# Kernel optimization log

Measured on AMD Instinct MI355X. Metric: run time of the kernel, lower is better.

The kernel has to match this reference:

```python
import jax, jax.numpy as jnp
import numpy as np

B, N, D, H, DK, DV, HID, L = 64, 512, 128, 8, 16, 16, 512, 3


def _attention(xq, xk, xv, Wq, Wk, Wv, Wo, mask=None):
    b, nq, _ = xq.shape
    nk = xk.shape[1]
    dk = Wq.shape[1] // H
    dv = Wv.shape[1] // H
    qs = (xq @ Wq).reshape(b, nq, H, dk).transpose(0, 2, 1, 3)   # [b,H,nq,dk]
    ks = (xk @ Wk).reshape(b, nk, H, dk).transpose(0, 2, 1, 3)   # [b,H,nk,dk]
    vs = (xv @ Wv).reshape(b, nk, H, dv).transpose(0, 2, 1, 3)   # [b,H,nk,dv]
    u = jnp.einsum('bhqd,bhkd->bhqk', qs, ks) / (float(dk) ** 0.5)
    if mask is not None:
        u = jnp.where(mask[:, None, None, :], -jnp.inf, u)
    a = jax.nn.softmax(u, axis=-1)
    att = jnp.einsum('bhqk,bhkd->bhqd', a, vs).transpose(0, 2, 1, 3).reshape(b, nq, H * dv)
    return att @ Wo


def _ln(x, g, b):
    mu = x.mean(-1, keepdims=True)
    var = ((x - mu) ** 2).mean(-1, keepdims=True)
    return (x - mu) / jnp.sqrt(var + 1e-6) * g + b


def setup_inputs() -> dict:
    key = jax.random.key(0)
    ks = jax.random.split(key, 32)
    s = 0.02
    def rn(k, shape):
        return jax.random.normal(k, shape, jnp.float32) * s
    return {
        'problems': jax.random.normal(ks[0], (B, N, 2), jnp.float32),
        'embed_W': rn(ks[1], (2, D)),
        'embed_b': jnp.zeros((D,), jnp.float32),
        'enc_Wq': rn(ks[2], (L, D, H * DK)),
        'enc_Wk': rn(ks[3], (L, D, H * DK)),
        'enc_Wv': rn(ks[4], (L, D, H * DV)),
        'enc_Wo': rn(ks[5], (L, H * DV, D)),
        'enc_ln1_g': jnp.ones((L, D), jnp.float32),
        'enc_ln1_b': jnp.zeros((L, D), jnp.float32),
        'enc_ff_W1': rn(ks[6], (L, D, HID)),
        'enc_ff_b1': jnp.zeros((L, HID), jnp.float32),
        'enc_ff_W2': rn(ks[7], (L, HID, D)),
        'enc_ff_b2': jnp.zeros((L, D), jnp.float32),
        'enc_ln2_g': jnp.ones((L, D), jnp.float32),
        'enc_ln2_b': jnp.zeros((L, D), jnp.float32),
        'graph_W': rn(ks[8], (D, D)),
        'node_W': rn(ks[9], (D, D)),
        'dec_Wq': rn(ks[10], (3 * D, H * DK)),
        'dec_Wk': rn(ks[11], (D, H * DK)),
        'dec_Wv': rn(ks[12], (D, H * DV)),
        'dec_Wo': rn(ks[13], (H * DV, D)),
        'W_v_f': jax.random.uniform(ks[14], (1, 1, D), jnp.float32),
        'W_v_l': jax.random.uniform(ks[15], (1, 1, D), jnp.float32),
    }


def reference(problems, embed_W, embed_b, enc_Wq, enc_Wk, enc_Wv, enc_Wo,
              enc_ln1_g, enc_ln1_b, enc_ff_W1, enc_ff_b1, enc_ff_W2, enc_ff_b2,
              enc_ln2_g, enc_ln2_b, graph_W, node_W,
              dec_Wq, dec_Wk, dec_Wv, dec_Wo, W_v_f, W_v_l):
    # --- encoder ---
    x = problems @ embed_W + embed_b
    for i in range(L):
        x = _ln(x + _attention(x, x, x, enc_Wq[i], enc_Wk[i], enc_Wv[i], enc_Wo[i]),
                enc_ln1_g[i], enc_ln1_b[i])
        h = jax.nn.relu(x @ enc_ff_W1[i] + enc_ff_b1[i]) @ enc_ff_W2[i] + enc_ff_b2[i]
        x = _ln(x + h, enc_ln2_g[i], enc_ln2_b[i])
    node_context = x                                             # [B,N,D]
    graph_context = node_context.mean(axis=1, keepdims=True) @ graph_W  # [B,1,D]
    k_node = node_context @ node_W                               # loop-invariant, hoisted
    first0 = jnp.broadcast_to(W_v_f, (B, 1, D))
    last0 = jnp.broadcast_to(W_v_l, (B, 1, D))
    mask0 = jnp.zeros((B, N), bool)
    step_keys = jax.random.split(jax.random.key(42), N)
    batch_idx = jnp.arange(B)

    def step(carry, inp):
        mask, last, first = carry
        i, k = inp
        cq = jnp.concatenate([graph_context, last, first], axis=-1)   # [B,1,3D]
        q = _attention(cq, node_context, node_context, dec_Wq, dec_Wk, dec_Wv, dec_Wo, mask)  # [B,1,D]
        logits = jnp.einsum('bqd,bnd->bqn', q, k_node)[:, 0, :] / (float(D) ** 0.5)
        logits = jnp.where(mask, -jnp.inf, jnp.tanh(logits) * 10.0)
        actions = jax.random.categorical(k, logits)                   # [B]
        probs = jax.nn.softmax(logits, axis=-1)
        p = jnp.take_along_axis(probs, actions[:, None], axis=1)[:, 0]
        mask = mask.at[batch_idx, actions].set(True)
        # faithful to original: gather index is [1,B,D], so it reads batch 0's node_context
        new_last = node_context[0][actions][:, None, :]               # [B,1,D]
        first = jnp.where(i == 0, new_last, first)
        return (mask, new_last, first), (p, actions)

    _, (probs_seq, actions_seq) = jax.lax.scan(
        step, (mask0, last0, first0), (jnp.arange(N), step_keys))
    return probs_seq, actions_seq
```

## Files before the change

### kernel.cpp

```cpp
#include <hip/hip_runtime.h>


#define NEGINF (-__builtin_huge_valf())
#define TINYF 1.17549435e-38f

__device__ __forceinline__ unsigned rotl32(unsigned v, int r) {
  return (v << r) | (v >> (32 - r));
}

__device__ __forceinline__ void threefry2x32(unsigned k0, unsigned k1,
                                             unsigned& x0, unsigned& x1) {
  unsigned k2 = k0 ^ k1 ^ 0x1BD11BDAu;
  x0 += k0; x1 += k1;
#define TF_R(r) { x0 += x1; x1 = rotl32(x1, (r)); x1 ^= x0; }
  TF_R(13) TF_R(15) TF_R(26) TF_R(6)
  x0 += k1; x1 += k2 + 1u;
  TF_R(17) TF_R(29) TF_R(16) TF_R(24)
  x0 += k2; x1 += k0 + 2u;
  TF_R(13) TF_R(15) TF_R(26) TF_R(6)
  x0 += k0; x1 += k1 + 3u;
  TF_R(17) TF_R(29) TF_R(16) TF_R(24)
  x0 += k1; x1 += k2 + 4u;
  TF_R(13) TF_R(15) TF_R(26) TF_R(6)
  x0 += k2; x1 += k0 + 5u;
#undef TF_R
}

__device__ __forceinline__ float4 f4fma(float s, float4 v, float4 a) {
  a.x += s * v.x; a.y += s * v.y; a.z += s * v.z; a.w += s * v.w; return a;
}

__global__ __launch_bounds__(256) void k_embed(const float* __restrict__ P,
                                               const float* __restrict__ eW,
                                               const float* __restrict__ eb,
                                               float* __restrict__ X) {
  int idx = blockIdx.x * 256 + threadIdx.x;
  int row = idx >> 7, d = idx & 127;
  X[idx] = P[row * 2] * eW[d] + P[row * 2 + 1] * eW[128 + d] + eb[d];
}

__global__ __launch_bounds__(256) void k_gemm128(const float* __restrict__ A,
                                                 const float* __restrict__ W,
                                                 const float* __restrict__ R,
                                                 float* __restrict__ C, int M) {
  __shared__ float As[16][129];
  __shared__ float Ws[128][17];
  const int tx = threadIdx.x & 15, ty = threadIdx.x >> 4;
  const int row0 = blockIdx.x * 16, col0 = blockIdx.y * 16;
  for (int idx = threadIdx.x; idx < 2048; idx += 256) {
    int r = idx >> 7, k = idx & 127;
    As[r][k] = (row0 + r < M) ? A[(size_t)(row0 + r) * 128 + k] : 0.0f;
    int kk = idx >> 4, c = idx & 15;
    Ws[kk][c] = W[(size_t)kk * 128 + col0 + c];
  }
  __syncthreads();
  float acc = 0.0f;
#pragma unroll 8
  for (int k = 0; k < 128; ++k) acc += As[ty][k] * Ws[k][tx];
  const int row = row0 + ty, col = col0 + tx;
  if (row < M) {
    if (R) acc += R[(size_t)row * 128 + col];
    C[(size_t)row * 128 + col] = acc;
  }
}

#define GEP_BIAS 1
#define GEP_RELU 2
#define GEP_ADDR 4
#define GEP_ACC  8
#define GEP_TST  16
#define GEP_WT   32

__global__ __launch_bounds__(256, 2) void k_gemm64(
    const float* __restrict__ A, int lda,
    const float* __restrict__ W, int ldw,
    const float* __restrict__ bias,
    const float* __restrict__ R,
    float* __restrict__ C, int ldc,
    int K, int flags) {
  __shared__ float AsT[128 * 68];
  __shared__ float Bs[128 * 68];
  const int t = threadIdx.x;
  const int tx = t & 15, ty = t >> 4;
  const int row0 = blockIdx.x * 64, col0 = blockIdx.y * 64;
  float4 acc[4];
  acc[0] = acc[1] = acc[2] = acc[3] = make_float4(0.f, 0.f, 0.f, 0.f);

  for (int K0 = 0; K0 < K; K0 += 128) {
    if (K0) __syncthreads();
#pragma unroll
    for (int j = 0; j < 8; ++j) {
      int idx = t + j * 256;
      int r = idx & 63, kq = idx >> 6;
      float4 v = *(const float4*)&A[(size_t)(row0 + r) * lda + K0 + kq * 4];
      AsT[(kq * 4 + 0) * 68 + r] = v.x;
      AsT[(kq * 4 + 1) * 68 + r] = v.y;
      AsT[(kq * 4 + 2) * 68 + r] = v.z;
      AsT[(kq * 4 + 3) * 68 + r] = v.w;
    }
    if (flags & GEP_WT) {
#pragma unroll
      for (int j = 0; j < 8; ++j) {
        int idx = t + j * 256;
        int cc = idx & 63, kq = idx >> 6;
        float4 v = *(const float4*)&W[(size_t)(col0 + cc) * ldw + K0 + kq * 4];
        Bs[(kq * 4 + 0) * 68 + cc] = v.x;
        Bs[(kq * 4 + 1) * 68 + cc] = v.y;
        Bs[(kq * 4 + 2) * 68 + cc] = v.z;
        Bs[(kq * 4 + 3) * 68 + cc] = v.w;
      }
    } else {
#pragma unroll
      for (int j = 0; j < 8; ++j) {
        int idx = t + j * 256;
        int c4 = idx & 15, k = idx >> 4;
        *(float4*)&Bs[k * 68 + c4 * 4] =
            *(const float4*)&W[(size_t)(K0 + k) * ldw + col0 + c4 * 4];
      }
    }
    __syncthreads();
#pragma unroll 8
    for (int k = 0; k < 128; ++k) {
      float4 av = *(const float4*)&AsT[k * 68 + ty * 4];
      float4 bv = *(const float4*)&Bs[k * 68 + tx * 4];
      acc[0] = f4fma(av.x, bv, acc[0]);
      acc[1] = f4fma(av.y, bv, acc[1]);
      acc[2] = f4fma(av.z, bv, acc[2]);
      acc[3] = f4fma(av.w, bv, acc[3]);
    }
  }

  if (flags & GEP_TST) {
    __syncthreads();
    float* CtT = AsT;
#pragma unroll
    for (int i2 = 0; i2 < 4; ++i2) {
      CtT[(tx * 4 + 0) * 68 + ty * 4 + i2] = ((const float*)&acc[i2])[0];
      CtT[(tx * 4 + 1) * 68 + ty * 4 + i2] = ((const float*)&acc[i2])[1];
      CtT[(tx * 4 + 2) * 68 + ty * 4 + i2] = ((const float*)&acc[i2])[2];
      CtT[(tx * 4 + 3) * 68 + ty * 4 + i2] = ((const float*)&acc[i2])[3];
    }
    __syncthreads();
    for (int j = 0; j < 16; ++j) {
      int idx = t + j * 256;
      int n = idx & 63, c = idx >> 6;
      int grow = row0 + n;
      C[(size_t)(grow >> 9) * 65536 + (size_t)(col0 + c) * 512 + (grow & 511)] =
          CtT[c * 68 + n];
    }
  } else {
#pragma unroll
    for (int i2 = 0; i2 < 4; ++i2) {
      const int row = row0 + ty * 4 + i2, col = col0 + tx * 4;
      float4 v = acc[i2];
      if (flags & GEP_BIAS) {
        float4 b4 = *(const float4*)&bias[col];
        v.x += b4.x; v.y += b4.y; v.z += b4.z; v.w += b4.w;
      }
      if (flags & GEP_RELU) {
        v.x = fmaxf(v.x, 0.f); v.y = fmaxf(v.y, 0.f);
        v.z = fmaxf(v.z, 0.f); v.w = fmaxf(v.w, 0.f);
      }
      if (flags & GEP_ADDR) {
        float4 r4 = *(const float4*)&R[(size_t)row * ldc + col];
        v.x += r4.x; v.y += r4.y; v.z += r4.z; v.w += r4.w;
      }
      if (flags & GEP_ACC) {
        float4 c4 = *(const float4*)&C[(size_t)row * ldc + col];
        v.x += c4.x; v.y += c4.y; v.z += c4.z; v.w += c4.w;
      }
      *(float4*)&C[(size_t)row * ldc + col] = v;
    }
  }
}

__global__ __launch_bounds__(512, 2) void k_attn_enc(const float* __restrict__ Q,
                                                     const float* __restrict__ K,
                                                     const float* __restrict__ V,
                                                     float* __restrict__ O) {
  const int b = blockIdx.x >> 3, h = blockIdx.x & 7;
  const int t = threadIdx.x, l = t & 63, w = t >> 6;
  __shared__ float4 Vs4[512][5];
  __shared__ float S[32][516];
  __shared__ float Qs[32][16];
  __shared__ float invr[32];
  const size_t base = (size_t)b * 512 * 128 + (size_t)h * 16;
  float4 k0, k1, k2, k3;
  {
    const float4* kr = reinterpret_cast<const float4*>(K + base + (size_t)t * 128);
    k0 = kr[0]; k1 = kr[1]; k2 = kr[2]; k3 = kr[3];
  }
  for (int idx = t; idx < 2048; idx += 512) {
    int n = idx >> 2, c = idx & 3;
    Vs4[n][c] = reinterpret_cast<const float4*>(V + base + (size_t)n * 128)[c];
  }
  __syncthreads();
  const float* vsf = reinterpret_cast<const float*>(Vs4);
  for (int qt = 0; qt < 16; ++qt) {
    { int qr = t >> 4, d = t & 15;
      Qs[qr][d] = Q[base + (size_t)(qt * 32 + qr) * 128 + d]; }
    __syncthreads();
#pragma unroll 4
    for (int qi = 0; qi < 32; ++qi) {
      const float* qv = Qs[qi];
      float s = qv[0] * k0.x + qv[1] * k0.y + qv[2] * k0.z + qv[3] * k0.w
              + qv[4] * k1.x + qv[5] * k1.y + qv[6] * k1.z + qv[7] * k1.w
              + qv[8] * k2.x + qv[9] * k2.y + qv[10] * k2.z + qv[11] * k2.w
              + qv[12] * k3.x + qv[13] * k3.y + qv[14] * k3.z + qv[15] * k3.w;
      S[qi][t] = s * 0.25f;
    }
    __syncthreads();
    for (int r = 0; r < 4; ++r) {
      const int qi = w * 4 + r;
      float m = S[qi][l];
      for (int j = 1; j < 8; ++j) m = fmaxf(m, S[qi][l + 64 * j]);
      for (int o = 32; o; o >>= 1) m = fmaxf(m, __shfl_xor(m, o));
      float sum = 0.0f;
      for (int j = 0; j < 8; ++j) {
        float e = expf(S[qi][l + 64 * j] - m);
        S[qi][l + 64 * j] = e;
        sum += e;
      }
      for (int o = 32; o; o >>= 1) sum += __shfl_xor(sum, o);
      if (l == 0) invr[qi] = 1.0f / sum;
    }
    __syncthreads();
    {
      const int qi = t >> 4, d = t & 15;
      float acc = 0.0f;
      for (int n = 0; n < 512; ++n) acc += S[qi][n] * vsf[n * 20 + d];
      O[base + (size_t)(qt * 32 + qi) * 128 + d] = acc * invr[qi];
    }
  }
}

__global__ __launch_bounds__(256) void k_ln(const float* __restrict__ Y,
                                            const float* __restrict__ g,
                                            const float* __restrict__ bb,
                                            float* __restrict__ O, int M) {
  const int row = blockIdx.x * 4 + (threadIdx.x >> 6);
  const int l = threadIdx.x & 63;
  if (row >= M) return;
  const float* y = Y + (size_t)row * 128;
  float v0 = y[l], v1 = y[l + 64];
  float s = v0 + v1;
  for (int o = 32; o; o >>= 1) s += __shfl_xor(s, o);
  const float mu = s * (1.0f / 128.0f);
  float d0 = v0 - mu, d1 = v1 - mu;
  float q = d0 * d0 + d1 * d1;
  for (int o = 32; o; o >>= 1) q += __shfl_xor(q, o);
  const float sd = sqrtf(q * (1.0f / 128.0f) + 1e-6f);
  O[(size_t)row * 128 + l]      = d0 / sd * g[l] + bb[l];
  O[(size_t)row * 128 + l + 64] = d1 / sd * g[l + 64] + bb[l + 64];
}

__global__ __launch_bounds__(128) void k_mean(const float* __restrict__ X,
                                              float* __restrict__ NM) {
  const int b = blockIdx.x, d = threadIdx.x;
  float s = 0.0f;
  for (int n = 0; n < 512; ++n) s += X[((size_t)b * 512 + n) * 128 + d];
  NM[b * 128 + d] = s * (1.0f / 512.0f);
}

__global__ __launch_bounds__(512, 2) void k_decoder(
    const float* __restrict__ Kt, const float* __restrict__ Vt,
    const float* __restrict__ KnWT,
    const float* __restrict__ QG, const float* __restrict__ QL,
    const float* __restrict__ QF, const float* __restrict__ QL0,
    const float* __restrict__ QF0,
    float* __restrict__ out_probs, float* __restrict__ out_act) {
  const int b = blockIdx.x, t = threadIdx.x;
  const int l = t & 63, w = t >> 6, h = w;

  __shared__ float att_s[128];
  __shared__ float pv[8][64 * 17];
  __shared__ float l_lds[512];
  __shared__ uint2 keys[512];
  __shared__ float redZ[8]; __shared__ int redI[8];
  __shared__ float redM[8]; __shared__ float redD[8];

  {
    unsigned x0 = 0u, x1 = (unsigned)t;
    threefry2x32(0u, 42u, x0, x1);
    keys[t] = make_uint2(x0, x1);
  }
  __syncthreads();

  const float4* KtB = reinterpret_cast<const float4*>(Kt + (size_t)b * 65536);
  const float4* VtB = reinterpret_cast<const float4*>(Vt + (size_t)b * 65536);
  const float*  knB = KnWT + (size_t)b * 65536;

  float4 mk0 = make_float4(0.f, 0.f, 0.f, 0.f);
  float4 mk1 = make_float4(0.f, 0.f, 0.f, 0.f);
  float emask = 0.0f;
  int ap = 0, af = 0;

  for (int i = 0; i < 512; ++i) {
    float qval = 0.0f;
    if (l < 16) {
      const int c = h * 16 + l;
      float s_ = QG[b * 128 + c];
      s_ += (i == 0) ? QL0[c] : QL[(size_t)ap * 128 + c];
      s_ += (i == 0) ? QF0[c] : QF[(size_t)af * 128 + c];
      qval = s_;
    }
    float q[16];
#pragma unroll
    for (int d = 0; d < 16; ++d) q[d] = __shfl(qval, d);
    float4 a0 = make_float4(0.f, 0.f, 0.f, 0.f);
    float4 a1 = make_float4(0.f, 0.f, 0.f, 0.f);
#pragma unroll
    for (int d = 0; d < 16; ++d) {
      a0 = f4fma(q[d], KtB[(h * 16 + d) * 128 + l], a0);
      a1 = f4fma(q[d], KtB[(h * 16 + d) * 128 + 64 + l], a1);
    }
    float4 va[4], vb[4];
#pragma unroll
    for (int u = 0; u < 4; ++u) {
      va[u] = VtB[(h * 16 + u) * 128 + l];
      vb[u] = VtB[(h * 16 + u) * 128 + 64 + l];
    }
    float4 s0, s1;
    s0.x = a0.x * 0.25f + mk0.x;  s0.y = a0.y * 0.25f + mk0.y;
    s0.z = a0.z * 0.25f + mk0.z;  s0.w = a0.w * 0.25f + mk0.w;
    s1.x = a1.x * 0.25f + mk1.x;  s1.y = a1.y * 0.25f + mk1.y;
    s1.z = a1.z * 0.25f + mk1.z;  s1.w = a1.w * 0.25f + mk1.w;
    float mh = fmaxf(fmaxf(fmaxf(s0.x, s0.y), fmaxf(s0.z, s0.w)),
                     fmaxf(fmaxf(s1.x, s1.y), fmaxf(s1.z, s1.w)));
    for (int o = 32; o; o >>= 1) mh = fmaxf(mh, __shfl_xor(mh, o));
    float4 e0, e1;
    e0.x = expf(s0.x - mh); e0.y = expf(s0.y - mh);
    e0.z = expf(s0.z - mh); e0.w = expf(s0.w - mh);
    e1.x = expf(s1.x - mh); e1.y = expf(s1.y - mh);
    e1.z = expf(s1.z - mh); e1.w = expf(s1.w - mh);
    float sden = ((e0.x + e0.y) + (e0.z + e0.w)) + ((e1.x + e1.y) + (e1.z + e1.w));
    for (int o = 32; o; o >>= 1) sden += __shfl_xor(sden, o);
    const float inv = 1.0f / sden;
    float ps[16];
#pragma unroll
    for (int u = 0; u < 4; ++u) {
      ps[u] = e0.x * va[u].x + e0.y * va[u].y + e0.z * va[u].z + e0.w * va[u].w
            + e1.x * vb[u].x + e1.y * vb[u].y + e1.z * vb[u].z + e1.w * vb[u].w;
    }
#pragma unroll
    for (int dg = 1; dg < 4; ++dg) {
#pragma unroll
      for (int u = 0; u < 4; ++u) {
        va[u] = VtB[(h * 16 + dg * 4 + u) * 128 + l];
        vb[u] = VtB[(h * 16 + dg * 4 + u) * 128 + 64 + l];
      }
#pragma unroll
      for (int u = 0; u < 4; ++u) {
        ps[dg * 4 + u] = e0.x * va[u].x + e0.y * va[u].y + e0.z * va[u].z + e0.w * va[u].w
                       + e1.x * vb[u].x + e1.y * vb[u].y + e1.z * vb[u].z + e1.w * vb[u].w;
      }
    }
#pragma unroll
    for (int d = 0; d < 16; ++d) pv[w][l * 17 + d] = ps[d];
    asm volatile("s_waitcnt lgkmcnt(0)" ::: "memory");
    float sum = 0.0f;
#pragma unroll
    for (int j = 0; j < 16; ++j)
      sum += pv[w][((l >> 4) * 16 + j) * 17 + (l & 15)];
    sum += __shfl_xor(sum, 16);
    sum += __shfl_xor(sum, 32);
    if (l < 16) att_s[h * 16 + l] = sum * inv;
    __syncthreads();
    float lg, zv;
    {
      const float4* att4 = reinterpret_cast<const float4*>(att_s);
      const float* kc = knB + t;
      float acc = 0.0f, acc2 = 0.0f;
#pragma unroll 8
      for (int k4 = 0; k4 < 32; ++k4) {
        float4 av = att4[k4];
        acc  += av.x * kc[(size_t)(4 * k4 + 0) * 512];
        acc  += av.y * kc[(size_t)(4 * k4 + 1) * 512];
        acc2 += av.z * kc[(size_t)(4 * k4 + 2) * 512];
        acc2 += av.w * kc[(size_t)(4 * k4 + 3) * 512];
      }
      const float lraw = (acc + acc2) / 11.313708498984761f;
      lg = tanhf(lraw) * 10.0f + emask;
      l_lds[t] = lg;
      unsigned x0 = 0u, x1 = (unsigned)(b * 512 + t);
      const uint2 kk = keys[i];
      threefry2x32(kk.x, kk.y, x0, x1);
      const unsigned bits = x0 ^ x1;
      float f = __uint_as_float((bits >> 9) | 0x3f800000u) - 1.0f;
      f = f + TINYF;
      f = fmaxf(TINYF, f);
      zv = lg + (-logf(-logf(f)));
    }
    {
      float z = zv; int zi = t;
      float mm = lg;
      for (int o = 32; o; o >>= 1) {
        float oz = __shfl_xor(z, o); int oi = __shfl_xor(zi, o);
        if (oz > z || (oz == z && oi < zi)) { z = oz; zi = oi; }
        mm = fmaxf(mm, __shfl_xor(mm, o));
      }
      float e = expf(lg - mm);
      for (int o = 32; o; o >>= 1) e += __shfl_xor(e, o);
      if (l == 0) { redZ[w] = z; redI[w] = zi; redM[w] = mm; redD[w] = e; }
    }
    __syncthreads();
    float bz = redZ[0]; int a = redI[0]; float M = redM[0];
#pragma unroll
    for (int ww = 1; ww < 8; ++ww) {
      float oz = redZ[ww]; int oi = redI[ww];
      if (oz > bz || (oz == bz && oi < a)) { bz = oz; a = oi; }
      M = fmaxf(M, redM[ww]);
    }
    if (t == 0) {
      float den = 0.0f;
#pragma unroll
      for (int ww = 0; ww < 8; ++ww) {
        float mw = redM[ww];
        if (mw != NEGINF) den += redD[ww] * expf(mw - M);
      }
      out_probs[i * 64 + b] = expf(l_lds[a] - M) / den;
      out_act[i * 64 + b] = (float)a;
    }
    ap = a;
    if (i == 0) af = a;
    const int n0 = l << 2;
    mk0.x = (a == n0)       ? NEGINF : mk0.x;
    mk0.y = (a == n0 + 1)   ? NEGINF : mk0.y;
    mk0.z = (a == n0 + 2)   ? NEGINF : mk0.z;
    mk0.w = (a == n0 + 3)   ? NEGINF : mk0.w;
    mk1.x = (a == 256 + n0)     ? NEGINF : mk1.x;
    mk1.y = (a == 256 + n0 + 1) ? NEGINF : mk1.y;
    mk1.z = (a == 256 + n0 + 2) ? NEGINF : mk1.z;
    mk1.w = (a == 256 + n0 + 3) ? NEGINF : mk1.w;
    emask = (a == t) ? NEGINF : emask;
  }
}

extern "C" void kernel_launch(void* const* d_in, const int* in_sizes, int n_in,
                              void* d_out, int out_size, void* d_ws, size_t ws_size,
                              hipStream_t stream) {
  const float* problems = (const float*)d_in[0];
  const float* embed_W  = (const float*)d_in[1];
  const float* embed_b  = (const float*)d_in[2];
  const float* enc_Wq   = (const float*)d_in[3];
  const float* enc_Wk   = (const float*)d_in[4];
  const float* enc_Wv   = (const float*)d_in[5];
  const float* enc_Wo   = (const float*)d_in[6];
  const float* ln1g     = (const float*)d_in[7];
  const float* ln1b     = (const float*)d_in[8];
  const float* ffW1     = (const float*)d_in[9];
  const float* ffb1     = (const float*)d_in[10];
  const float* ffW2     = (const float*)d_in[11];
  const float* ffb2     = (const float*)d_in[12];
  const float* ln2g     = (const float*)d_in[13];
  const float* ln2b     = (const float*)d_in[14];
  const float* graph_W  = (const float*)d_in[15];
  const float* node_W   = (const float*)d_in[16];
  const float* dec_Wq   = (const float*)d_in[17];
  const float* dec_Wk   = (const float*)d_in[18];
  const float* dec_Wv   = (const float*)d_in[19];
  const float* dec_Wo   = (const float*)d_in[20];
  const float* W_v_f    = (const float*)d_in[21];
  const float* W_v_l    = (const float*)d_in[22];

  float* ws = (float*)d_ws;
  const size_t SZ = (size_t)64 * 512 * 128;
  float* X  = ws;
  float* Y  = ws + SZ;
  float* Qb = ws + 2 * SZ;
  float* Kb = ws + 3 * SZ;
  float* Vb = ws + 4 * SZ;
  float* NM = ws + 5 * SZ;
  float* GC = NM + 64 * 128;

  float* QG  = Y;
  float* QL  = Y + 8192;
  float* QF  = Y + 8192 + 65536;
  float* QL0 = Y + 8192 + 131072;
  float* QF0 = QL0 + 128;

  float* out       = (float*)d_out;
  float* out_probs = out;
  float* out_act   = out + 512 * 64;

  k_embed<<<16384, 256, 0, stream>>>(problems, embed_W, embed_b, X);

  for (int i = 0; i < 3; ++i) {
    const float* Wqi = enc_Wq + (size_t)i * 16384;
    const float* Wki = enc_Wk + (size_t)i * 16384;
    const float* Wvi = enc_Wv + (size_t)i * 16384;
    const float* Woi = enc_Wo + (size_t)i * 16384;
    k_gemm64<<<dim3(512, 2), 256, 0, stream>>>(X, 128, Wqi, 128, nullptr, nullptr, Qb, 128, 128, 0);
    k_gemm64<<<dim3(512, 2), 256, 0, stream>>>(X, 128, Wki, 128, nullptr, nullptr, Kb, 128, 128, 0);
    k_gemm64<<<dim3(512, 2), 256, 0, stream>>>(X, 128, Wvi, 128, nullptr, nullptr, Vb, 128, 128, 0);
    k_attn_enc<<<512, 512, 0, stream>>>(Qb, Kb, Vb, Y);
    k_gemm64<<<dim3(512, 2), 256, 0, stream>>>(Y, 128, Woi, 128, nullptr, X, Qb, 128, 128, GEP_ADDR);
    k_ln<<<8192, 256, 0, stream>>>(Qb, ln1g + i * 128, ln1b + i * 128, X, 32768);
    float* H = Kb;
    for (int half = 0; half < 2; ++half) {
      k_gemm64<<<dim3(512, 4), 256, 0, stream>>>(
          X, 128, ffW1 + (size_t)i * 65536 + half * 256, 512,
          ffb1 + i * 512 + half * 256, nullptr, H, 256, 128, GEP_BIAS | GEP_RELU);
      k_gemm64<<<dim3(512, 2), 256, 0, stream>>>(
          H, 256, ffW2 + (size_t)i * 65536 + (size_t)half * 32768, 128,
          ffb2 + i * 128, X, Y, 128, 256,
          half == 0 ? (GEP_BIAS | GEP_ADDR) : GEP_ACC);
    }
    k_ln<<<8192, 256, 0, stream>>>(Y, ln2g + i * 128, ln2b + i * 128, X, 32768);
  }

  k_mean<<<64, 128, 0, stream>>>(X, NM);
  k_gemm128<<<dim3(4, 8), 256, 0, stream>>>(NM, graph_W, nullptr, GC, 64);
  k_gemm128<<<dim3(4, 8), 256, 0, stream>>>(GC, dec_Wq, nullptr, QG, 64);
  k_gemm64<<<dim3(8, 2), 256, 0, stream>>>(X, 128, dec_Wq + 16384, 128, nullptr, nullptr, QL, 128, 128, 0);
  k_gemm64<<<dim3(8, 2), 256, 0, stream>>>(X, 128, dec_Wq + 32768, 128, nullptr, nullptr, QF, 128, 128, 0);
  k_gemm128<<<dim3(1, 8), 256, 0, stream>>>(W_v_l, dec_Wq + 16384, nullptr, QL0, 1);
  k_gemm128<<<dim3(1, 8), 256, 0, stream>>>(W_v_f, dec_Wq + 32768, nullptr, QF0, 1);
  k_gemm64<<<dim3(512, 2), 256, 0, stream>>>(X, 128, dec_Wk, 128, nullptr, nullptr, Qb, 128, 128, GEP_TST);
  k_gemm64<<<dim3(512, 2), 256, 0, stream>>>(X, 128, dec_Wv, 128, nullptr, nullptr, Kb, 128, 128, GEP_TST);
  k_gemm64<<<dim3(512, 2), 256, 0, stream>>>(X, 128, node_W, 128, nullptr, nullptr, Vb, 128, 128, 0);
  k_gemm64<<<dim3(512, 2), 256, 0, stream>>>(Vb, 128, dec_Wo, 128, nullptr, nullptr, X, 128, 128,
                                             GEP_WT | GEP_TST);

  k_decoder<<<64, 512, 0, stream>>>(Qb, Kb, X, QG, QL, QF, QL0, QF0,
                                    out_probs, out_act);
}
```

Baseline: 8.387 ms.

## Repack decoder node-key matrix into float4-interleaved layout and prefetch before barrier

A new repack kernel rewrites the transposed node-key matrix so that four consecutive feature rows for a node sit together as one float4. The decoder's logit dot product can then use 128-bit loads instead of scalar strided loads. The first 8 float4s are issued before the __syncthreads so their latency overlaps the barrier. The graph and first-node query terms are also hoisted into registers, which removes two global loads per step. The cost is one extra small kernel launch and more register pressure in a kernel capped by a launch bound of 2 blocks.

```diff
diff --git a/kernel.cpp b/kernel.cpp
--- a/kernel.cpp
+++ b/kernel.cpp
@@ -172,6 +172,15 @@
       *(float4*)&C[(size_t)row * ldc + col] = v;
     }
   }
+}
+
+__global__ __launch_bounds__(256) void k_repack4(const float* __restrict__ in,
+                                                 float* __restrict__ out) {
+  int idx = blockIdx.x * 256 + threadIdx.x;
+  int n = idx & 511, q = (idx >> 9) & 31, b = idx >> 14;
+  const float* ip = in + (size_t)b * 65536 + (size_t)(q * 4) * 512 + n;
+  float4 v = make_float4(ip[0], ip[512], ip[1024], ip[1536]);
+  *reinterpret_cast<float4*>(out + (size_t)b * 65536 + (size_t)q * 2048 + n * 4) = v;
 }
 
 __global__ __launch_bounds__(512, 2) void k_attn_enc(const float* __restrict__ Q,
@@ -264,7 +273,7 @@
 
 __global__ __launch_bounds__(512, 2) void k_decoder(
     const float* __restrict__ Kt, const float* __restrict__ Vt,
-    const float* __restrict__ KnWT,
+    const float* __restrict__ KnW4,
     const float* __restrict__ QG, const float* __restrict__ QL,
     const float* __restrict__ QF, const float* __restrict__ QL0,
     const float* __restrict__ QF0,
@@ -288,21 +297,23 @@
 
   const float4* KtB = reinterpret_cast<const float4*>(Kt + (size_t)b * 65536);
   const float4* VtB = reinterpret_cast<const float4*>(Vt + (size_t)b * 65536);
-  const float*  knB = KnWT + (size_t)b * 65536;
+  const float4* kn4 = reinterpret_cast<const float4*>(KnW4 + (size_t)b * 65536);
 
   float4 mk0 = make_float4(0.f, 0.f, 0.f, 0.f);
   float4 mk1 = make_float4(0.f, 0.f, 0.f, 0.f);
   float emask = 0.0f;
   int ap = 0, af = 0;
 
+  float qg = 0.0f, qf_r = 0.0f;
+  if (l < 16) qg = QG[b * 128 + h * 16 + l];
+
   for (int i = 0; i < 512; ++i) {
     float qval = 0.0f;
     if (l < 16) {
       const int c = h * 16 + l;
-      float s_ = QG[b * 128 + c];
-      s_ += (i == 0) ? QL0[c] : QL[(size_t)ap * 128 + c];
-      s_ += (i == 0) ? QF0[c] : QF[(size_t)af * 128 + c];
-      qval = s_;
+      const float ql_ = (i == 0) ? QL0[c] : QL[(size_t)ap * 128 + c];
+      const float qf_ = (i == 0) ? QF0[c] : qf_r;
+      qval = (qg + ql_) + qf_;
     }
     float q[16];
 #pragma unroll
@@ -365,19 +376,27 @@
     sum += __shfl_xor(sum, 16);
     sum += __shfl_xor(sum, 32);
     if (l < 16) att_s[h * 16 + l] = sum * inv;
+    float4 kq[8];
+#pragma unroll
+    for (int q4 = 0; q4 < 8; ++q4) kq[q4] = kn4[q4 * 512 + t];
     __syncthreads();
     float lg, zv;
     {
       const float4* att4 = reinterpret_cast<const float4*>(att_s);
-      const float* kc = knB + t;
       float acc = 0.0f, acc2 = 0.0f;
+#pragma unroll
+      for (int q4 = 0; q4 < 8; ++q4) {
+        const float4 av = att4[q4];
+        const float4 kv = kq[q4];
+        acc  += av.x * kv.x;  acc  += av.y * kv.y;
+        acc2 += av.z * kv.z;  acc2 += av.w * kv.w;
+      }
 #pragma unroll 8
-      for (int k4 = 0; k4 < 32; ++k4) {
-        float4 av = att4[k4];
-        acc  += av.x * kc[(size_t)(4 * k4 + 0) * 512];
-        acc  += av.y * kc[(size_t)(4 * k4 + 1) * 512];
-        acc2 += av.z * kc[(size_t)(4 * k4 + 2) * 512];
-        acc2 += av.w * kc[(size_t)(4 * k4 + 3) * 512];
+      for (int q4 = 8; q4 < 32; ++q4) {
+        const float4 av = att4[q4];
+        const float4 kv = kn4[q4 * 512 + t];
+        acc  += av.x * kv.x;  acc  += av.y * kv.y;
+        acc2 += av.z * kv.z;  acc2 += av.w * kv.w;
       }
       const float lraw = (acc + acc2) / 11.313708498984761f;
       lg = tanhf(lraw) * 10.0f + emask;
@@ -422,7 +441,10 @@
       out_act[i * 64 + b] = (float)a;
     }
     ap = a;
-    if (i == 0) af = a;
+    if (i == 0) {
+      af = a;
+      if (l < 16) qf_r = QF[(size_t)a * 128 + h * 16 + l];
+    }
     const int n0 = l << 2;
     mk0.x = (a == n0)       ? NEGINF : mk0.x;
     mk0.y = (a == n0 + 1)   ? NEGINF : mk0.y;
@@ -521,7 +543,8 @@
   k_gemm64<<<dim3(512, 2), 256, 0, stream>>>(X, 128, node_W, 128, nullptr, nullptr, Vb, 128, 128, 0);
   k_gemm64<<<dim3(512, 2), 256, 0, stream>>>(Vb, 128, dec_Wo, 128, nullptr, nullptr, X, 128, 128,
                                              GEP_WT | GEP_TST);
-
-  k_decoder<<<64, 512, 0, stream>>>(Qb, Kb, X, QG, QL, QF, QL0, QF0,
+  k_repack4<<<4096, 256, 0, stream>>>(X, Vb);
+
+  k_decoder<<<64, 512, 0, stream>>>(Qb, Kb, Vb, QG, QL, QF, QL0, QF0,
                                     out_probs, out_act);
 }
```

Result: slower. 10.01 ms (+19.3%).
